# Kernel optimization log

Measured on AMD Instinct MI355X. Metric: run time of the kernel, lower is better.

The kernel has to match this reference:

```python
import jax, jax.numpy as jnp
import numpy as np

B, N, F, H, M, EF, OUT = 256, 32, 40, 100, 100, 4, 128
MESSAGE_PASSES = 3


def setup_inputs() -> dict:
    key = jax.random.key(0)
    ks = jax.random.split(key, 8)
    # Deterministic ring graphs: node i <-> node (i+1)%N, one-hot bond type.
    # Every node has degree 2 -> static nonzero counts.
    rng = np.random.default_rng(0)
    edges = np.zeros((B, N, N, EF), np.float32)
    b = np.arange(B)[:, None]
    i = np.arange(N)[None, :]
    j = (i + 1) % N
    t = rng.integers(0, EF, size=(B, N))
    edges[b, i, j, t] = 1.0
    edges[b, j, i, t] = 1.0

    nodes = jax.random.normal(ks[0], (B, N, F), jnp.float32)

    def init(k, shape, fan):
        return jax.random.normal(k, shape, jnp.float32) / np.sqrt(fan).astype(np.float32)

    W_msg = init(ks[1], (M, H, EF), H)          # MNN edge-conditioned weights
    W_ih = init(ks[2], (3 * H, M), M)            # GRUCell input weights
    W_hh = init(ks[3], (3 * H, H), H)            # GRUCell hidden weights
    b_ih = jnp.zeros((3 * H,), jnp.float32)
    b_hh = jnp.zeros((3 * H,), jnp.float32)
    Wg = init(ks[4], (H + F, H), H + F)          # gather gate
    bg = jnp.zeros((H,), jnp.float32)
    We = init(ks[5], (H, H), H)                  # gather embed
    be = jnp.zeros((H,), jnp.float32)
    Wo = init(ks[6], (H, OUT), H)                # output head
    bo = jnp.zeros((OUT,), jnp.float32)

    return {
        "nodes": nodes, "edges": jnp.asarray(edges),
        "W_msg": W_msg, "W_ih": W_ih, "W_hh": W_hh, "b_ih": b_ih, "b_hh": b_hh,
        "Wg": Wg, "bg": bg, "We": We, "be": be, "Wo": Wo, "bo": bo,
        "n_edges": B * N * 2, "n_node_entries": B * N,
    }


def gru_cell(x, h, W_ih, W_hh, b_ih, b_hh):
    gi = x @ W_ih.T + b_ih
    gh = h @ W_hh.T + b_hh
    ir, iz, inn = jnp.split(gi, 3, axis=-1)
    hr, hz, hn = jnp.split(gh, 3, axis=-1)
    r = jax.nn.sigmoid(ir + hr)
    z = jax.nn.sigmoid(iz + hz)
    n = jnp.tanh(inn + r * hn)
    return (1.0 - z) * n + z * h


def reference(nodes, edges, W_msg, W_ih, W_hh, b_ih, b_hh, Wg, bg, We, be, Wo, bo,
              n_edges, n_node_entries):
    adjacency = jnp.sum(edges, axis=3)                      # (B, N, N)
    eb, en, eg = jnp.nonzero(adjacency, size=n_edges)       # edge-level indices
    nb, nn_ = jnp.nonzero(adjacency.sum(-1), size=n_node_entries)

    # Dense one-hot segment-sum matrix: (n_node_entries, n_edges)
    same = (nb[:, None] == eb) & (nn_[:, None] == en)
    msg_sum_mat = same.astype(jnp.float32)

    edge_batch_edges = edges[eb, en, eg, :]                 # (E, EF)

    hidden = jnp.zeros((B, N, H), jnp.float32).at[:, :, :F].set(nodes)
    node_h = hidden[nb, nn_, :]                             # (V, H)

    for _ in range(MESSAGE_PASSES):
        nghb_h = hidden[eb, eg, :]                          # (E, H)
        # MNN message: sum_f edges[e,f] * W_msg[m,h,f] * nghb[e,h]
        message_terms = jnp.einsum('ef,mhf,eh->em', edge_batch_edges, W_msg, nghb_h)
        messages = msg_sum_mat @ message_terms              # (V, M) dense one-hot matmul
        node_h = gru_cell(messages, node_h, W_ih, W_hh, b_ih, b_hh)
        hidden = hidden.at[nb, nn_, :].set(node_h)

    node_mask = (adjacency.sum(-1) != 0).astype(jnp.float32)  # (B, N)
    cat = jnp.concatenate([hidden, nodes], axis=-1)           # (B, N, H+F)
    gate = jax.nn.sigmoid(cat @ Wg + bg)
    emb = gate * (hidden @ We + be)
    graph_emb = jnp.sum(emb * node_mask[..., None], axis=1)   # (B, H)
    return graph_emb @ Wo + bo                                # (B, OUT)
```

## Files before the change

### kernel.cpp

```cpp
#include <hip/hip_runtime.h>
#include <cstddef>
#include <cstdint>

#define B_   256
#define N_   32
#define F_   40
#define H_   100
#define OUT_ 128
#define TB   1024
#define XCS  168
#define XMS  136
#define AWS  40
#define ZSP  40
#define NBLK 343
#define NLO  63

using bf16x8 = __attribute__((ext_vector_type(8))) short;
using f32x4  = __attribute__((ext_vector_type(4))) float;

#define MFMA(a,b,c) __builtin_amdgcn_mfma_f32_16x16x32_bf16((a),(b),(c),0,0,0)

__device__ __forceinline__ float sigmoidf_(float x){ return 1.0f/(1.0f+__expf(-x)); }
__device__ __forceinline__ float tanhf_(float x){
  float e = __expf(2.0f*x);
  return 1.0f - 2.0f/(e+1.0f);
}
__device__ __forceinline__ float bf2f(short s){ return __uint_as_float(((uint32_t)(uint16_t)s)<<16); }
__device__ __forceinline__ short f2bf(float x){
  uint32_t u = __float_as_uint(x);
  return (short)((u + 0x7FFFu + ((u>>16)&1u))>>16);
}
__device__ __forceinline__ void bsplit(float x, short& hi, short& lo){
  hi = f2bf(x);
  lo = f2bf(x - bf2f(hi));
}

__global__ void prep_frags4(const float* __restrict__ Wmsg,
                            const float* __restrict__ Wih,
                            const float* __restrict__ Whh,
                            const float* __restrict__ Wg,
                            const float* __restrict__ We,
                            short* __restrict__ AFhi,
                            short* __restrict__ AFlo){
  int slot = blockIdx.x*blockDim.x + threadIdx.x;
  if (slot >= NBLK*512) return;
  int blk = slot>>9, r = slot&511, lane = r>>3, jj = r&7;
  int m = lane&15, q = lane>>4, kl = q*8+jj;
  float v = 0.0f;
  if (blk < 112){
    int t = blk/28, rem = blk%28, jmt = rem>>2, ks = rem&3;
    int mg = jmt*16+m, h = ks*32+kl;
    if (mg<100 && h<100) v = Wmsg[(mg*100+h)*4 + t];
    AFhi[slot] = f2bf(v);
  } else if (blk < 280){
    int bb = blk-112, mat = bb/28, rem = bb%28, jmt = rem>>2, ks = rem&3;
    int mg = jmt*16+m, k = ks*32+kl;
    if (mg<100 && k<100)
      v = (mat<3) ? Wih[(mat*100+mg)*100+k] : Whh[((mat-3)*100+mg)*100+k];
    AFhi[slot] = f2bf(v);
  } else if (blk < 315){
    int bb = blk-280, jmt = bb/5, ks = bb%5;
    int mg = jmt*16+m, k = ks*32+kl;
    if (mg<100 && k<140) v = Wg[k*100+mg];
    short hi,lo; bsplit(v,hi,lo);
    AFhi[slot] = hi;
    AFlo[(size_t)(blk-280)*512 + r] = lo;
  } else {
    int bb = blk-315, jmt = bb>>2, ks = bb&3;
    int mg = jmt*16+m, k = ks*32+kl;
    if (mg<100 && k<100) v = We[k*100+mg];
    short hi,lo; bsplit(v,hi,lo);
    AFhi[slot] = hi;
    AFlo[(size_t)(blk-280)*512 + r] = lo;
  }
}

__global__ __launch_bounds__(TB, 4) void mpnn_mfma(
    const float* __restrict__ nodes, const float* __restrict__ edges,
    const short* __restrict__ AFhi, const short* __restrict__ AFlo,
    const float* __restrict__ b_ih, const float* __restrict__ b_hh,
    const float* __restrict__ bg, const float* __restrict__ be,
    const float* __restrict__ Wo, const float* __restrict__ bo,
    float* __restrict__ out){
  const int b = blockIdx.x;
  const int tid = threadIdx.x;
  const int lane = tid & 63;
  const int w = tid >> 6;

  __shared__ short XcH[32*XCS];
  __shared__ short XmH[32*XMS];
  __shared__ short Aw[4][32*AWS];
  __shared__ short Zs[14*16*ZSP];
  __shared__ float sh_ge[H_];
  __shared__ float sh_part[4][OUT_];
  __shared__ int   sh_msk[N_];

  for (int i=tid;i<(32*XCS)/2;i+=TB){ ((int*)XcH)[i]=0; }
  for (int i=tid;i<(32*XMS)/2;i+=TB){ ((int*)XmH)[i]=0; }
  if (tid < H_) sh_ge[tid]=0.0f;
  __syncthreads();

  {
    int n = tid>>5, g = tid&31;
    const float4 ev = *(const float4*)(edges + (((size_t)b*N_+n)*N_+g)*4);
    float adj = ev.x+ev.y+ev.z+ev.w;
    unsigned long long bal = __ballot(adj != 0.0f);
    if (lane == 0)  sh_msk[n] = ((int)(bal & 0xFFFFFFFFull)) != 0;
    if (lane == 32) sh_msk[n] = ((int)(bal >> 32)) != 0;
    Aw[0][n*AWS+g] = f2bf(ev.x);
    Aw[1][n*AWS+g] = f2bf(ev.y);
    Aw[2][n*AWS+g] = f2bf(ev.z);
    Aw[3][n*AWS+g] = f2bf(ev.w);
  }
  for (int p=tid; p<N_*F_; p+=TB){
    int n = p/F_, f = p%F_;
    float x = nodes[((size_t)b*N_+n)*F_ + f];
    short hi = f2bf(x);
    XcH[n*XCS+f]=hi;
    XcH[n*XCS+100+f]=hi;
  }

  const int jmt = w>>1, nt = w&1;
  const bool task = (w < 14);
  const int nrow = nt*16 + (lane&15);
  const int boff = (lane>>4)*8;
  const int rowbase = jmt*16 + (lane>>4)*4;
  const int zb = w*16*ZSP;
  const int zcol = lane&15;
  const int zrow = (lane>>4)*4;

  float hst[4] = {0.f,0.f,0.f,0.f};
  if (task){
#pragma unroll
    for (int r=0;r<4;++r){
      int row = rowbase + r;
      if (row < F_) hst[r] = nodes[((size_t)b*N_+nrow)*F_ + row];
    }
  }
  __syncthreads();

  for (int pass=0; pass<3; ++pass){
    f32x4 Ch0=(f32x4)0.0f, Ch1=(f32x4)0.0f, Ch2=(f32x4)0.0f;
    if (task){
      {
        const short* pb = XcH + nrow*XCS + boff;
        bf16x8 b0 = *(const bf16x8*)(pb);
        bf16x8 b1 = *(const bf16x8*)(pb+32);
        bf16x8 b2 = *(const bf16x8*)(pb+64);
        bf16x8 b3 = *(const bf16x8*)(pb+96);
        const short* pa = AFhi + ((size_t)(112 + 3*28 + jmt*4))*512 + lane*8;
        {
          bf16x8 a0=*(const bf16x8*)(pa),      a1=*(const bf16x8*)(pa+512);
          bf16x8 a2=*(const bf16x8*)(pa+1024), a3=*(const bf16x8*)(pa+1536);
          Ch0 = MFMA(a0,b0,Ch0); Ch0 = MFMA(a1,b1,Ch0);
          Ch0 = MFMA(a2,b2,Ch0); Ch0 = MFMA(a3,b3,Ch0);
        }
        pa += 28*512;
        {
          bf16x8 a0=*(const bf16x8*)(pa),      a1=*(const bf16x8*)(pa+512);
          bf16x8 a2=*(const bf16x8*)(pa+1024), a3=*(const bf16x8*)(pa+1536);
          Ch1 = MFMA(a0,b0,Ch1); Ch1 = MFMA(a1,b1,Ch1);
          Ch1 = MFMA(a2,b2,Ch1); Ch1 = MFMA(a3,b3,Ch1);
        }
        pa += 28*512;
        {
          bf16x8 a0=*(const bf16x8*)(pa),      a1=*(const bf16x8*)(pa+512);
          bf16x8 a2=*(const bf16x8*)(pa+1024), a3=*(const bf16x8*)(pa+1536);
          Ch2 = MFMA(a0,b0,Ch2); Ch2 = MFMA(a1,b1,Ch2);
          Ch2 = MFMA(a2,b2,Ch2); Ch2 = MFMA(a3,b3,Ch2);
        }
      }
      {
        f32x4 Cm=(f32x4)0.0f;
#pragma unroll 1
        for (int t=0;t<4;++t){
          const short* pa = AFhi + ((size_t)(t*28 + jmt*4))*512 + lane*8;
          bf16x8 a0 = *(const bf16x8*)(pa);
          bf16x8 a1 = *(const bf16x8*)(pa+512);
          bf16x8 a2 = *(const bf16x8*)(pa+1024);
          bf16x8 a3 = *(const bf16x8*)(pa+1536);
          const short* pg0 = XcH + (lane&15)*XCS + boff;
          const short* pg1 = pg0 + 16*XCS;
          f32x4 Z0=(f32x4)0.0f, Z1=(f32x4)0.0f;
          Z0 = MFMA(a0, *(const bf16x8*)(pg0),    Z0);
          Z0 = MFMA(a1, *(const bf16x8*)(pg0+32), Z0);
          Z0 = MFMA(a2, *(const bf16x8*)(pg0+64), Z0);
          Z0 = MFMA(a3, *(const bf16x8*)(pg0+96), Z0);
          Z1 = MFMA(a0, *(const bf16x8*)(pg1),    Z1);
          Z1 = MFMA(a1, *(const bf16x8*)(pg1+32), Z1);
          Z1 = MFMA(a2, *(const bf16x8*)(pg1+64), Z1);
          Z1 = MFMA(a3, *(const bf16x8*)(pg1+96), Z1);
#pragma unroll
          for (int r=0;r<4;++r){
            Zs[zb + (zrow+r)*ZSP + zcol]      = f2bf(Z0[r]);
            Zs[zb + (zrow+r)*ZSP + zcol + 16] = f2bf(Z1[r]);
          }
          bf16x8 az = *(const bf16x8*)&Zs[zb + (lane&15)*ZSP + boff];
          bf16x8 bt = *(const bf16x8*)&Aw[t][nrow*AWS + boff];
          Cm = MFMA(az, bt, Cm);
        }
        if (rowbase < 100){
          short4 pk;
          pk.x = f2bf(Cm[0]); pk.y = f2bf(Cm[1]);
          pk.z = f2bf(Cm[2]); pk.w = f2bf(Cm[3]);
          *(short4*)&XmH[nrow*XMS + rowbase] = pk;
        }
      }
    }
    __syncthreads();
    if (task){
      f32x4 Ci0=(f32x4)0.0f, Ci1=(f32x4)0.0f, Ci2=(f32x4)0.0f;
      {
        const short* pb = XmH + nrow*XMS + boff;
        bf16x8 b0 = *(const bf16x8*)(pb);
        bf16x8 b1 = *(const bf16x8*)(pb+32);
        bf16x8 b2 = *(const bf16x8*)(pb+64);
        bf16x8 b3 = *(const bf16x8*)(pb+96);
        const short* pa = AFhi + ((size_t)(112 + jmt*4))*512 + lane*8;
        {
          bf16x8 a0=*(const bf16x8*)(pa),      a1=*(const bf16x8*)(pa+512);
          bf16x8 a2=*(const bf16x8*)(pa+1024), a3=*(const bf16x8*)(pa+1536);
          Ci0 = MFMA(a0,b0,Ci0); Ci0 = MFMA(a1,b1,Ci0);
          Ci0 = MFMA(a2,b2,Ci0); Ci0 = MFMA(a3,b3,Ci0);
        }
        pa += 28*512;
        {
          bf16x8 a0=*(const bf16x8*)(pa),      a1=*(const bf16x8*)(pa+512);
          bf16x8 a2=*(const bf16x8*)(pa+1024), a3=*(const bf16x8*)(pa+1536);
          Ci1 = MFMA(a0,b0,Ci1); Ci1 = MFMA(a1,b1,Ci1);
          Ci1 = MFMA(a2,b2,Ci1); Ci1 = MFMA(a3,b3,Ci1);
        }
        pa += 28*512;
        {
          bf16x8 a0=*(const bf16x8*)(pa),      a1=*(const bf16x8*)(pa+512);
          bf16x8 a2=*(const bf16x8*)(pa+1024), a3=*(const bf16x8*)(pa+1536);
          Ci2 = MFMA(a0,b0,Ci2); Ci2 = MFMA(a1,b1,Ci2);
          Ci2 = MFMA(a2,b2,Ci2); Ci2 = MFMA(a3,b3,Ci2);
        }
      }
      if (rowbase < 100){
        bool msk = sh_msk[nrow] != 0;
        short4 pk;
#pragma unroll
        for (int r=0;r<4;++r){
          int row = rowbase + r;
          float ho = hst[r];
          float rr = sigmoidf_(Ci0[r]+Ch0[r] + b_ih[row]     + b_hh[row]);
          float zz = sigmoidf_(Ci1[r]+Ch1[r] + b_ih[100+row] + b_hh[100+row]);
          float nn = tanhf_(Ci2[r] + b_ih[200+row] + rr*(Ch2[r] + b_hh[200+row]));
          float hnew = (1.0f-zz)*nn + zz*ho;
          if (!msk) hnew = ho;
          hst[r] = hnew;
          ((short*)&pk)[r] = f2bf(hnew);
        }
        *(short4*)&XcH[nrow*XCS + rowbase] = pk;
      }
    }
    __syncthreads();
  }

  f32x4 Cg=(f32x4)0.0f, Ce=(f32x4)0.0f;
  if (task){
    const short* pb = XcH + nrow*XCS + boff;
    bf16x8 b0 = *(const bf16x8*)(pb);
    bf16x8 b1 = *(const bf16x8*)(pb+32);
    bf16x8 b2 = *(const bf16x8*)(pb+64);
    bf16x8 b3 = *(const bf16x8*)(pb+96);
    bf16x8 b4 = *(const bf16x8*)(pb+128);
    {
      const short* ph = AFhi + ((size_t)(280 + jmt*5))*512 + lane*8;
      const short* pl = AFlo + ((size_t)(jmt*5))*512 + lane*8;
      Cg = MFMA(*(const bf16x8*)(ph),      b0, Cg);
      Cg = MFMA(*(const bf16x8*)(pl),      b0, Cg);
      Cg = MFMA(*(const bf16x8*)(ph+512),  b1, Cg);
      Cg = MFMA(*(const bf16x8*)(pl+512),  b1, Cg);
      Cg = MFMA(*(const bf16x8*)(ph+1024), b2, Cg);
      Cg = MFMA(*(const bf16x8*)(pl+1024), b2, Cg);
      Cg = MFMA(*(const bf16x8*)(ph+1536), b3, Cg);
      Cg = MFMA(*(const bf16x8*)(pl+1536), b3, Cg);
      Cg = MFMA(*(const bf16x8*)(ph+2048), b4, Cg);
      Cg = MFMA(*(const bf16x8*)(pl+2048), b4, Cg);
    }
    {
      const short* ph = AFhi + ((size_t)(315 + jmt*4))*512 + lane*8;
      const short* pl = AFlo + ((size_t)(35 + jmt*4))*512 + lane*8;
      Ce = MFMA(*(const bf16x8*)(ph),      b0, Ce);
      Ce = MFMA(*(const bf16x8*)(pl),      b0, Ce);
      Ce = MFMA(*(const bf16x8*)(ph+512),  b1, Ce);
      Ce = MFMA(*(const bf16x8*)(pl+512),  b1, Ce);
      Ce = MFMA(*(const bf16x8*)(ph+1024), b2, Ce);
      Ce = MFMA(*(const bf16x8*)(pl+1024), b2, Ce);
      Ce = MFMA(*(const bf16x8*)(ph+1536), b3, Ce);
      Ce = MFMA(*(const bf16x8*)(pl+1536), b3, Ce);
    }
    bool msk = sh_msk[nrow] != 0;
#pragma unroll
    for (int r=0;r<4;++r){
      int row = rowbase + r;
      float v = 0.0f;
      if (row<100){
        float gate = sigmoidf_(Cg[r] + bg[row]);
        float emb  = gate*(Ce[r] + be[row]);
        v = msk ? emb : 0.0f;
      }
      v += __shfl_xor(v, 1);
      v += __shfl_xor(v, 2);
      v += __shfl_xor(v, 4);
      v += __shfl_xor(v, 8);
      if (row<100 && (lane&15)==0) atomicAdd(&sh_ge[row], v);
    }
  }
  __syncthreads();
  if (tid < 512){
    int o = tid & 127, q = tid >> 7;
    float s = 0.0f;
    int k0 = 25*q;
#pragma unroll 5
    for (int k=k0; k<k0+25; ++k) s += sh_ge[k]*Wo[k*OUT_+o];
    sh_part[q][o] = s;
  }
  __syncthreads();
  if (tid < OUT_){
    out[(size_t)b*OUT_ + tid] = bo[tid] + sh_part[0][tid] + sh_part[1][tid]
                              + sh_part[2][tid] + sh_part[3][tid];
  }
}

extern "C" void kernel_launch(void* const* d_in, const int* in_sizes, int n_in,
                              void* d_out, int out_size, void* d_ws, size_t ws_size,
                              hipStream_t stream){
  const float* nodes = (const float*)d_in[0];
  const float* edges = (const float*)d_in[1];
  const float* W_msg = (const float*)d_in[2];
  const float* W_ih  = (const float*)d_in[3];
  const float* W_hh  = (const float*)d_in[4];
  const float* b_ih  = (const float*)d_in[5];
  const float* b_hh  = (const float*)d_in[6];
  const float* Wg    = (const float*)d_in[7];
  const float* bg    = (const float*)d_in[8];
  const float* We    = (const float*)d_in[9];
  const float* be    = (const float*)d_in[10];
  const float* Wo    = (const float*)d_in[11];
  const float* bo    = (const float*)d_in[12];

  short* AFhi = (short*)d_ws;
  short* AFlo = AFhi + (size_t)NBLK*512;

  prep_frags4<<<(NBLK*512 + 255)/256, 256, 0, stream>>>(W_msg, W_ih, W_hh, Wg, We,
                                                        AFhi, AFlo);
  mpnn_mfma<<<B_, TB, 0, stream>>>(nodes, edges, AFhi, AFlo, b_ih, b_hh, bg, be,
                                   Wo, bo, (float*)d_out);
}
```

Before: 123.0 us.

## Halve block size and have each wave cover both node tiles with register-held GRU weights

Block size drops from 1024 to 512 threads, so 7 task waves each handle both 16-node column tiles instead of 14 waves handling one each. GRU input and hidden weight fragments and biases are loaded into registers once before the pass loop instead of being re-read from global memory every pass. The edge-conditioned message stage is unrolled so the W_msg fragments are reused across both node tiles, with a larger per-wave shared scratch. This cuts repeated global weight loads, but raises register pressure (about 96 VGPRs of weight fragments per lane) and halves the wave-level parallelism inside each block.

```diff
diff --git a/kernel.cpp b/kernel.cpp
--- a/kernel.cpp
+++ b/kernel.cpp
@@ -7,7 +7,7 @@
 #define F_   40
 #define H_   100
 #define OUT_ 128
-#define TB   1024
+#define TB   512
 #define XCS  168
 #define XMS  136
 #define AWS  40
@@ -75,7 +75,7 @@
   }
 }
 
-__global__ __launch_bounds__(TB, 4) void mpnn_mfma(
+__global__ __launch_bounds__(TB, 2) void mpnn_mfma(
     const float* __restrict__ nodes, const float* __restrict__ edges,
     const short* __restrict__ AFhi, const short* __restrict__ AFlo,
     const float* __restrict__ b_ih, const float* __restrict__ b_hh,
@@ -90,7 +90,7 @@
   __shared__ short XcH[32*XCS];
   __shared__ short XmH[32*XMS];
   __shared__ short Aw[4][32*AWS];
-  __shared__ short Zs[14*16*ZSP];
+  __shared__ short Zs[7*4*16*ZSP];
   __shared__ float sh_ge[H_];
   __shared__ float sh_part[4][OUT_];
   __shared__ int   sh_msk[N_];
@@ -100,8 +100,8 @@
   if (tid < H_) sh_ge[tid]=0.0f;
   __syncthreads();
 
-  {
-    int n = tid>>5, g = tid&31;
+  for (int e=tid; e<N_*N_; e+=TB){
+    int n = e>>5, g = e&31;
     const float4 ev = *(const float4*)(edges + (((size_t)b*N_+n)*N_+g)*4);
     float adj = ev.x+ev.y+ev.z+ev.w;
     unsigned long long bal = __ballot(adj != 0.0f);
@@ -120,189 +120,221 @@
     XcH[n*XCS+100+f]=hi;
   }
 
-  const int jmt = w>>1, nt = w&1;
-  const bool task = (w < 14);
-  const int nrow = nt*16 + (lane&15);
-  const int boff = (lane>>4)*8;
-  const int rowbase = jmt*16 + (lane>>4)*4;
-  const int zb = w*16*ZSP;
-  const int zcol = lane&15;
-  const int zrow = (lane>>4)*4;
-
-  float hst[4] = {0.f,0.f,0.f,0.f};
+  const int jmt = w;
+  const bool task = (w < 7);
+  const int c16 = lane & 15;
+  const int q   = lane >> 4;
+  const int boff = q*8;
+  const int rowbase = jmt*16 + q*4;
+  const int n0 = c16, n1 = 16 + c16;
+
+  bf16x8 Ai[3][4], Ah[3][4];
+  if (task){
+#pragma unroll
+    for (int mat=0; mat<3; ++mat){
+#pragma unroll
+      for (int ks=0; ks<4; ++ks){
+        Ai[mat][ks] = *(const bf16x8*)(AFhi + ((size_t)(112 + mat*28 + jmt*4 + ks))*512 + lane*8);
+        Ah[mat][ks] = *(const bf16x8*)(AFhi + ((size_t)(112 + (3+mat)*28 + jmt*4 + ks))*512 + lane*8);
+      }
+    }
+  }
+  float bi0[4],bi1[4],bi2[4],bh0[4],bh1[4],bh2[4];
   if (task){
 #pragma unroll
     for (int r=0;r<4;++r){
       int row = rowbase + r;
-      if (row < F_) hst[r] = nodes[((size_t)b*N_+nrow)*F_ + row];
+      bool ok = row < 100;
+      bi0[r] = ok ? b_ih[row]       : 0.0f;
+      bi1[r] = ok ? b_ih[100+row]   : 0.0f;
+      bi2[r] = ok ? b_ih[200+row]   : 0.0f;
+      bh0[r] = ok ? b_hh[row]       : 0.0f;
+      bh1[r] = ok ? b_hh[100+row]   : 0.0f;
+      bh2[r] = ok ? b_hh[200+row]   : 0.0f;
+    }
+  }
+
+  float hst0[4]={0.f,0.f,0.f,0.f}, hst1[4]={0.f,0.f,0.f,0.f};
+  if (task){
+#pragma unroll
+    for (int r=0;r<4;++r){
+      int row = rowbase + r;
+      if (row < F_){
+        hst0[r] = nodes[((size_t)b*N_+n0)*F_ + row];
+        hst1[r] = nodes[((size_t)b*N_+n1)*F_ + row];
+      }
     }
   }
   __syncthreads();
 
   for (int pass=0; pass<3; ++pass){
-    f32x4 Ch0=(f32x4)0.0f, Ch1=(f32x4)0.0f, Ch2=(f32x4)0.0f;
+    f32x4 Chh[3][2];
+#pragma unroll
+    for (int m3=0;m3<3;++m3){ Chh[m3][0]=(f32x4)0.0f; Chh[m3][1]=(f32x4)0.0f; }
     if (task){
-      {
-        const short* pb = XcH + nrow*XCS + boff;
-        bf16x8 b0 = *(const bf16x8*)(pb);
-        bf16x8 b1 = *(const bf16x8*)(pb+32);
-        bf16x8 b2 = *(const bf16x8*)(pb+64);
-        bf16x8 b3 = *(const bf16x8*)(pb+96);
-        const short* pa = AFhi + ((size_t)(112 + 3*28 + jmt*4))*512 + lane*8;
-        {
-          bf16x8 a0=*(const bf16x8*)(pa),      a1=*(const bf16x8*)(pa+512);
-          bf16x8 a2=*(const bf16x8*)(pa+1024), a3=*(const bf16x8*)(pa+1536);
-          Ch0 = MFMA(a0,b0,Ch0); Ch0 = MFMA(a1,b1,Ch0);
-          Ch0 = MFMA(a2,b2,Ch0); Ch0 = MFMA(a3,b3,Ch0);
-        }
-        pa += 28*512;
-        {
-          bf16x8 a0=*(const bf16x8*)(pa),      a1=*(const bf16x8*)(pa+512);
-          bf16x8 a2=*(const bf16x8*)(pa+1024), a3=*(const bf16x8*)(pa+1536);
-          Ch1 = MFMA(a0,b0,Ch1); Ch1 = MFMA(a1,b1,Ch1);
-          Ch1 = MFMA(a2,b2,Ch1); Ch1 = MFMA(a3,b3,Ch1);
-        }
-        pa += 28*512;
-        {
-          bf16x8 a0=*(const bf16x8*)(pa),      a1=*(const bf16x8*)(pa+512);
-          bf16x8 a2=*(const bf16x8*)(pa+1024), a3=*(const bf16x8*)(pa+1536);
-          Ch2 = MFMA(a0,b0,Ch2); Ch2 = MFMA(a1,b1,Ch2);
-          Ch2 = MFMA(a2,b2,Ch2); Ch2 = MFMA(a3,b3,Ch2);
-        }
-      }
-      {
-        f32x4 Cm=(f32x4)0.0f;
-#pragma unroll 1
-        for (int t=0;t<4;++t){
+      const short* pb0 = XcH + n0*XCS + boff;
+      const short* pb1 = XcH + n1*XCS + boff;
+      bf16x8 x0[4], x1[4];
+#pragma unroll
+      for (int ks=0;ks<4;++ks){
+        x0[ks] = *(const bf16x8*)(pb0 + ks*32);
+        x1[ks] = *(const bf16x8*)(pb1 + ks*32);
+      }
+      f32x4 Cm0=(f32x4)0.0f, Cm1=(f32x4)0.0f;
+#pragma unroll
+      for (int th=0; th<2; ++th){
+        f32x4 Za[2][2];
+#pragma unroll
+        for (int u=0;u<2;++u){
+          int t = th*2+u;
           const short* pa = AFhi + ((size_t)(t*28 + jmt*4))*512 + lane*8;
           bf16x8 a0 = *(const bf16x8*)(pa);
           bf16x8 a1 = *(const bf16x8*)(pa+512);
           bf16x8 a2 = *(const bf16x8*)(pa+1024);
           bf16x8 a3 = *(const bf16x8*)(pa+1536);
-          const short* pg0 = XcH + (lane&15)*XCS + boff;
-          const short* pg1 = pg0 + 16*XCS;
-          f32x4 Z0=(f32x4)0.0f, Z1=(f32x4)0.0f;
-          Z0 = MFMA(a0, *(const bf16x8*)(pg0),    Z0);
-          Z0 = MFMA(a1, *(const bf16x8*)(pg0+32), Z0);
-          Z0 = MFMA(a2, *(const bf16x8*)(pg0+64), Z0);
-          Z0 = MFMA(a3, *(const bf16x8*)(pg0+96), Z0);
-          Z1 = MFMA(a0, *(const bf16x8*)(pg1),    Z1);
-          Z1 = MFMA(a1, *(const bf16x8*)(pg1+32), Z1);
-          Z1 = MFMA(a2, *(const bf16x8*)(pg1+64), Z1);
-          Z1 = MFMA(a3, *(const bf16x8*)(pg1+96), Z1);
+          Za[u][0]=(f32x4)0.0f; Za[u][1]=(f32x4)0.0f;
+          Za[u][0]=MFMA(a0,x0[0],Za[u][0]); Za[u][0]=MFMA(a1,x0[1],Za[u][0]);
+          Za[u][0]=MFMA(a2,x0[2],Za[u][0]); Za[u][0]=MFMA(a3,x0[3],Za[u][0]);
+          Za[u][1]=MFMA(a0,x1[0],Za[u][1]); Za[u][1]=MFMA(a1,x1[1],Za[u][1]);
+          Za[u][1]=MFMA(a2,x1[2],Za[u][1]); Za[u][1]=MFMA(a3,x1[3],Za[u][1]);
+        }
+#pragma unroll
+        for (int u=0;u<2;++u){
+          int t = th*2+u;
+          int zb = (w*4+t)*16*ZSP;
 #pragma unroll
           for (int r=0;r<4;++r){
-            Zs[zb + (zrow+r)*ZSP + zcol]      = f2bf(Z0[r]);
-            Zs[zb + (zrow+r)*ZSP + zcol + 16] = f2bf(Z1[r]);
+            Zs[zb + (q*4+r)*ZSP + c16]      = f2bf(Za[u][0][r]);
+            Zs[zb + (q*4+r)*ZSP + c16 + 16] = f2bf(Za[u][1][r]);
           }
-          bf16x8 az = *(const bf16x8*)&Zs[zb + (lane&15)*ZSP + boff];
-          bf16x8 bt = *(const bf16x8*)&Aw[t][nrow*AWS + boff];
-          Cm = MFMA(az, bt, Cm);
-        }
-        if (rowbase < 100){
-          short4 pk;
-          pk.x = f2bf(Cm[0]); pk.y = f2bf(Cm[1]);
-          pk.z = f2bf(Cm[2]); pk.w = f2bf(Cm[3]);
-          *(short4*)&XmH[nrow*XMS + rowbase] = pk;
+        }
+#pragma unroll
+        for (int u=0;u<2;++u){
+          int t = th*2+u;
+          int zb = (w*4+t)*16*ZSP;
+          bf16x8 az  = *(const bf16x8*)&Zs[zb + c16*ZSP + boff];
+          bf16x8 bt0 = *(const bf16x8*)&Aw[t][n0*AWS + boff];
+          bf16x8 bt1 = *(const bf16x8*)&Aw[t][n1*AWS + boff];
+          Cm0 = MFMA(az, bt0, Cm0);
+          Cm1 = MFMA(az, bt1, Cm1);
+        }
+      }
+      if (rowbase < 100){
+        short4 pk0, pk1;
+        pk0.x=f2bf(Cm0[0]); pk0.y=f2bf(Cm0[1]); pk0.z=f2bf(Cm0[2]); pk0.w=f2bf(Cm0[3]);
+        pk1.x=f2bf(Cm1[0]); pk1.y=f2bf(Cm1[1]); pk1.z=f2bf(Cm1[2]); pk1.w=f2bf(Cm1[3]);
+        *(short4*)&XmH[n0*XMS + rowbase] = pk0;
+        *(short4*)&XmH[n1*XMS + rowbase] = pk1;
+      }
+#pragma unroll
+      for (int m3=0;m3<3;++m3){
+#pragma unroll
+        for (int ks=0;ks<4;++ks){
+          Chh[m3][0] = MFMA(Ah[m3][ks], x0[ks], Chh[m3][0]);
+          Chh[m3][1] = MFMA(Ah[m3][ks], x1[ks], Chh[m3][1]);
         }
       }
     }
     __syncthreads();
     if (task){
-      f32x4 Ci0=(f32x4)0.0f, Ci1=(f32x4)0.0f, Ci2=(f32x4)0.0f;
-      {
-        const short* pb = XmH + nrow*XMS + boff;
-        bf16x8 b0 = *(const bf16x8*)(pb);
-        bf16x8 b1 = *(const bf16x8*)(pb+32);
-        bf16x8 b2 = *(const bf16x8*)(pb+64);
-        bf16x8 b3 = *(const bf16x8*)(pb+96);
-        const short* pa = AFhi + ((size_t)(112 + jmt*4))*512 + lane*8;
-        {
-          bf16x8 a0=*(const bf16x8*)(pa),      a1=*(const bf16x8*)(pa+512);
-          bf16x8 a2=*(const bf16x8*)(pa+1024), a3=*(const bf16x8*)(pa+1536);
-          Ci0 = MFMA(a0,b0,Ci0); Ci0 = MFMA(a1,b1,Ci0);
-          Ci0 = MFMA(a2,b2,Ci0); Ci0 = MFMA(a3,b3,Ci0);
-        }
-        pa += 28*512;
-        {
-          bf16x8 a0=*(const bf16x8*)(pa),      a1=*(const bf16x8*)(pa+512);
-          bf16x8 a2=*(const bf16x8*)(pa+1024), a3=*(const bf16x8*)(pa+1536);
-          Ci1 = MFMA(a0,b0,Ci1); Ci1 = MFMA(a1,b1,Ci1);
-          Ci1 = MFMA(a2,b2,Ci1); Ci1 = MFMA(a3,b3,Ci1);
-        }
-        pa += 28*512;
-        {
-          bf16x8 a0=*(const bf16x8*)(pa),      a1=*(const bf16x8*)(pa+512);
-          bf16x8 a2=*(const bf16x8*)(pa+1024), a3=*(const bf16x8*)(pa+1536);
-          Ci2 = MFMA(a0,b0,Ci2); Ci2 = MFMA(a1,b1,Ci2);
-          Ci2 = MFMA(a2,b2,Ci2); Ci2 = MFMA(a3,b3,Ci2);
+      const short* pm0 = XmH + n0*XMS + boff;
+      const short* pm1 = XmH + n1*XMS + boff;
+      bf16x8 m0f[4], m1f[4];
+#pragma unroll
+      for (int ks=0;ks<4;++ks){
+        m0f[ks] = *(const bf16x8*)(pm0 + ks*32);
+        m1f[ks] = *(const bf16x8*)(pm1 + ks*32);
+      }
+      f32x4 Ci[3][2];
+#pragma unroll
+      for (int m3=0;m3<3;++m3){ Ci[m3][0]=(f32x4)0.0f; Ci[m3][1]=(f32x4)0.0f; }
+#pragma unroll
+      for (int m3=0;m3<3;++m3){
+#pragma unroll
+        for (int ks=0;ks<4;++ks){
+          Ci[m3][0] = MFMA(Ai[m3][ks], m0f[ks], Ci[m3][0]);
+          Ci[m3][1] = MFMA(Ai[m3][ks], m1f[ks], Ci[m3][1]);
         }
       }
       if (rowbase < 100){
-        bool msk = sh_msk[nrow] != 0;
-        short4 pk;
+        bool k0 = sh_msk[n0] != 0, k1 = sh_msk[n1] != 0;
+        short4 pk0, pk1;
 #pragma unroll
         for (int r=0;r<4;++r){
-          int row = rowbase + r;
-          float ho = hst[r];
-          float rr = sigmoidf_(Ci0[r]+Ch0[r] + b_ih[row]     + b_hh[row]);
-          float zz = sigmoidf_(Ci1[r]+Ch1[r] + b_ih[100+row] + b_hh[100+row]);
-          float nn = tanhf_(Ci2[r] + b_ih[200+row] + rr*(Ch2[r] + b_hh[200+row]));
-          float hnew = (1.0f-zz)*nn + zz*ho;
-          if (!msk) hnew = ho;
-          hst[r] = hnew;
-          ((short*)&pk)[r] = f2bf(hnew);
-        }
-        *(short4*)&XcH[nrow*XCS + rowbase] = pk;
+          {
+            float ho = hst0[r];
+            float rr = sigmoidf_(Ci[0][0][r]+Chh[0][0][r] + bi0[r] + bh0[r]);
+            float zz = sigmoidf_(Ci[1][0][r]+Chh[1][0][r] + bi1[r] + bh1[r]);
+            float nn = tanhf_(Ci[2][0][r] + bi2[r] + rr*(Chh[2][0][r] + bh2[r]));
+            float hnew = (1.0f-zz)*nn + zz*ho;
+            if (!k0) hnew = ho;
+            hst0[r] = hnew;
+            ((short*)&pk0)[r] = f2bf(hnew);
+          }
+          {
+            float ho = hst1[r];
+            float rr = sigmoidf_(Ci[0][1][r]+Chh[0][1][r] + bi0[r] + bh0[r]);
+            float zz = sigmoidf_(Ci[1][1][r]+Chh[1][1][r] + bi1[r] + bh1[r]);
+            float nn = tanhf_(Ci[2][1][r] + bi2[r] + rr*(Chh[2][1][r] + bh2[r]));
+            float hnew = (1.0f-zz)*nn + zz*ho;
+            if (!k1) hnew = ho;
+            hst1[r] = hnew;
+            ((short*)&pk1)[r] = f2bf(hnew);
+          }
+        }
+        *(short4*)&XcH[n0*XCS + rowbase] = pk0;
+        *(short4*)&XcH[n1*XCS + rowbase] = pk1;
       }
     }
     __syncthreads();
   }
 
-  f32x4 Cg=(f32x4)0.0f, Ce=(f32x4)0.0f;
   if (task){
-    const short* pb = XcH + nrow*XCS + boff;
-    bf16x8 b0 = *(const bf16x8*)(pb);
-    bf16x8 b1 = *(const bf16x8*)(pb+32);
-    bf16x8 b2 = *(const bf16x8*)(pb+64);
-    bf16x8 b3 = *(const bf16x8*)(pb+96);
-    bf16x8 b4 = *(const bf16x8*)(pb+128);
+    const short* pb0 = XcH + n0*XCS + boff;
+    const short* pb1 = XcH + n1*XCS + boff;
+    bf16x8 rb0[5], rb1[5];
+#pragma unroll
+    for (int ks=0;ks<5;++ks){
+      rb0[ks] = *(const bf16x8*)(pb0 + ks*32);
+      rb1[ks] = *(const bf16x8*)(pb1 + ks*32);
+    }
+    f32x4 Cg0=(f32x4)0.0f, Cg1=(f32x4)0.0f, Ce0=(f32x4)0.0f, Ce1=(f32x4)0.0f;
     {
       const short* ph = AFhi + ((size_t)(280 + jmt*5))*512 + lane*8;
       const short* pl = AFlo + ((size_t)(jmt*5))*512 + lane*8;
-      Cg = MFMA(*(const bf16x8*)(ph),      b0, Cg);
-      Cg = MFMA(*(const bf16x8*)(pl),      b0, Cg);
-      Cg = MFMA(*(const bf16x8*)(ph+512),  b1, Cg);
-      Cg = MFMA(*(const bf16x8*)(pl+512),  b1, Cg);
-      Cg = MFMA(*(const bf16x8*)(ph+1024), b2, Cg);
-      Cg = MFMA(*(const bf16x8*)(pl+1024), b2, Cg);
-      Cg = MFMA(*(const bf16x8*)(ph+1536), b3, Cg);
-      Cg = MFMA(*(const bf16x8*)(pl+1536), b3, Cg);
-      Cg = MFMA(*(const bf16x8*)(ph+2048), b4, Cg);
-      Cg = MFMA(*(const bf16x8*)(pl+2048), b4, Cg);
+#pragma unroll
+      for (int ks=0;ks<5;++ks){
+        bf16x8 ah = *(const bf16x8*)(ph + ks*512);
+        bf16x8 al = *(const bf16x8*)(pl + ks*512);
+        Cg0 = MFMA(ah, rb0[ks], Cg0); Cg0 = MFMA(al, rb0[ks], Cg0);
+        Cg1 = MFMA(ah, rb1[ks], Cg1); Cg1 = MFMA(al, rb1[ks], Cg1);
+      }
     }
     {
       const short* ph = AFhi + ((size_t)(315 + jmt*4))*512 + lane*8;
       const short* pl = AFlo + ((size_t)(35 + jmt*4))*512 + lane*8;
-      Ce = MFMA(*(const bf16x8*)(ph),      b0, Ce);
-      Ce = MFMA(*(const bf16x8*)(pl),      b0, Ce);
-      Ce = MFMA(*(const bf16x8*)(ph+512),  b1, Ce);
-      Ce = MFMA(*(const bf16x8*)(pl+512),  b1, Ce);
-      Ce = MFMA(*(const bf16x8*)(ph+1024), b2, Ce);
-      Ce = MFMA(*(const bf16x8*)(pl+1024), b2, Ce);
-      Ce = MFMA(*(const bf16x8*)(ph+1536), b3, Ce);
-      Ce = MFMA(*(const bf16x8*)(pl+1536), b3, Ce);
-    }
-    bool msk = sh_msk[nrow] != 0;
+#pragma unroll
+      for (int ks=0;ks<4;++ks){
+        bf16x8 ah = *(const bf16x8*)(ph + ks*512);
+        bf16x8 al = *(const bf16x8*)(pl + ks*512);
+        Ce0 = MFMA(ah, rb0[ks], Ce0); Ce0 = MFMA(al, rb0[ks], Ce0);
+        Ce1 = MFMA(ah, rb1[ks], Ce1); Ce1 = MFMA(al, rb1[ks], Ce1);
+      }
+    }
+    bool k0 = sh_msk[n0] != 0, k1 = sh_msk[n1] != 0;
 #pragma unroll
     for (int r=0;r<4;++r){
       int row = rowbase + r;
-      float v = 0.0f;
+      float v0 = 0.0f, v1 = 0.0f;
       if (row<100){
-        float gate = sigmoidf_(Cg[r] + bg[row]);
-        float emb  = gate*(Ce[r] + be[row]);
-        v = msk ? emb : 0.0f;
-      }
+        float g0 = sigmoidf_(Cg0[r] + bg[row]);
+        float g1 = sigmoidf_(Cg1[r] + bg[row]);
+        float e0 = g0*(Ce0[r] + be[row]);
+        float e1 = g1*(Ce1[r] + be[row]);
+        v0 = k0 ? e0 : 0.0f;
+        v1 = k1 ? e1 : 0.0f;
+      }
+      float v = v0 + v1;
       v += __shfl_xor(v, 1);
       v += __shfl_xor(v, 2);
       v += __shfl_xor(v, 4);
@@ -311,13 +343,13 @@
     }
   }
   __syncthreads();
-  if (tid < 512){
-    int o = tid & 127, q = tid >> 7;
+  {
+    int o = tid & 127, qq = tid >> 7;
     float s = 0.0f;
-    int k0 = 25*q;
+    int k0 = 25*qq;
 #pragma unroll 5
     for (int k=k0; k<k0+25; ++k) s += sh_ge[k]*Wo[k*OUT_+o];
-    sh_part[q][o] = s;
+    sh_part[qq][o] = s;
   }
   __syncthreads();
   if (tid < OUT_){
```

Measured after the change: 108.9 us. 1.13x faster.
